# Optimization experiments

Measured on AMD Instinct MI355X. Metric: run time of the kernel, lower is better.

The kernel has to match this reference:

```python
import jax, jax.numpy as jnp
import numpy as np

R, N, F_IN, F_OUT = 8, 40000, 128, 128
E = 160000  # edges per relation


def setup_inputs() -> dict:
    key = jax.random.key(0)
    ks = jax.random.split(key, 10)
    ent_mat = jax.random.normal(ks[0], (N, F_IN), dtype=jnp.float32)
    rel_mat = jax.random.normal(ks[1], (R, F_IN), dtype=jnp.float32)
    edge_src = jax.random.randint(ks[2], (R, E), 0, N, dtype=jnp.int32)
    edge_dst = jax.random.randint(ks[3], (R, E), 0, N, dtype=jnp.int32)
    edge_val = jax.random.uniform(ks[4], (R, E), dtype=jnp.float32)
    # learned params (xavier-ish scale)
    s_e = (6.0 / (F_IN + F_OUT)) ** 0.5
    weight_ent = jax.random.uniform(ks[5], (F_IN, F_OUT), minval=-s_e, maxval=s_e, dtype=jnp.float32)
    proj_w1 = jax.random.uniform(ks[6], (F_IN, F_OUT), minval=-s_e, maxval=s_e, dtype=jnp.float32)
    proj_b1 = jnp.zeros((F_OUT,), dtype=jnp.float32)
    s_2 = (6.0 / (F_OUT + 1)) ** 0.5
    proj_w2 = jax.random.uniform(ks[7], (F_OUT, 1), minval=-s_2, maxval=s_2, dtype=jnp.float32)
    return {"ent_mat": ent_mat, "rel_mat": rel_mat, "edge_src": edge_src,
            "edge_dst": edge_dst, "edge_val": edge_val, "weight_ent": weight_ent,
            "proj_w1": proj_w1, "proj_b1": proj_b1, "proj_w2": proj_w2}


def reference(ent_mat, rel_mat, edge_src, edge_dst, edge_val, weight_ent, proj_w1, proj_b1, proj_w2):
    # Per-relation SpMM: supports[r] = A_r @ ent_mat, via edge-list segment-sum.
    seg = (jnp.arange(R, dtype=jnp.int32)[:, None] * N + edge_src).reshape(-1)  # [R*E]
    msgs = edge_val.reshape(-1, 1) * ent_mat[edge_dst.reshape(-1)]              # [R*E, F_IN]
    supports = jax.ops.segment_sum(msgs, seg, num_segments=R * N).reshape(R, N, F_IN)
    # Relation gate: sigmoid(Linear(Tanh(Linear(rel_mat))))
    h = jnp.tanh(rel_mat @ proj_w1 + proj_b1)      # [R, F_OUT]
    alpha = jax.nn.sigmoid(h @ proj_w2)            # [R, 1]
    alpha = alpha[:, None, :]                      # [R, 1, 1]
    # Weighted matmul + sum over relations (fused via einsum)
    ent_output = jnp.einsum('rnf,fo->no', supports * alpha, weight_ent)  # [N, F_OUT]
    return (ent_output, rel_mat)
```

## Files before the change

kernel.cpp:

```cpp
#include <hip/hip_runtime.h>

#define R_ 8
#define N_ 40000
#define F_ 128
#define E_ 160000
#define NE (R_ * E_)
#define NBUK 625
#define CAP 2560
#define FBLK 320
#define FCHUNK 4000
#define RELCHUNKS (E_ / FCHUNK)

typedef unsigned short ushort;
typedef unsigned int uint;
typedef __attribute__((ext_vector_type(8))) short bf16x8;
typedef __attribute__((ext_vector_type(4))) float f32x4;

__device__ __forceinline__ ushort f2bf(float x) {
    uint u = __float_as_uint(x);
    return (ushort)((u + 0x7fffu + ((u >> 16) & 1u)) >> 16);
}

__global__ __launch_bounds__(256) void fused_prep(
        const float* __restrict__ ent, const float* __restrict__ W,
        ushort* __restrict__ proj,
        const int* __restrict__ esrc,
        const float* __restrict__ rel, float* __restrict__ out_tail,
        const float* __restrict__ w1, const float* __restrict__ b1,
        const float* __restrict__ w2, float* __restrict__ alpha,
        int* __restrict__ hist) {
    __shared__ float smem[64 * F_];
    const int t = threadIdx.x;
    const int b = blockIdx.x;
    if (b < 625) {
        ushort* Wt = (ushort*)smem;
#pragma unroll
        for (int p = 0; p < 16; ++p) {
            int k = p * 8 + (t >> 5);
            int c4 = (t & 31) * 4;
            float4 wv = *(const float4*)&W[k * F_ + c4];
#pragma unroll
            for (int i = 0; i < 4; ++i) {
                int col = c4 + i;
                float v = (i == 0) ? wv.x : (i == 1) ? wv.y : (i == 2) ? wv.z : wv.w;
                Wt[col * F_ + ((((k >> 3) ^ (col & 7)) << 3) | (k & 7))] = f2bf(v);
            }
        }
        __syncthreads();
        const int wv_ = t >> 6;
        const int lane = t & 63;
        const int m = lane & 15;
        const int q = (lane >> 4) & 3;
        const int row0 = b * 64 + wv_ * 16;
        bf16x8 afrag[4];
        const float* arow = ent + (size_t)(row0 + m) * F_;
#pragma unroll
        for (int kc = 0; kc < 4; ++kc) {
            float4 a0 = *(const float4*)&arow[kc * 32 + q * 8];
            float4 a1 = *(const float4*)&arow[kc * 32 + q * 8 + 4];
            bf16x8 a;
            a[0] = (short)f2bf(a0.x); a[1] = (short)f2bf(a0.y);
            a[2] = (short)f2bf(a0.z); a[3] = (short)f2bf(a0.w);
            a[4] = (short)f2bf(a1.x); a[5] = (short)f2bf(a1.y);
            a[6] = (short)f2bf(a1.z); a[7] = (short)f2bf(a1.w);
            afrag[kc] = a;
        }
        f32x4 acc[8];
#pragma unroll
        for (int ct = 0; ct < 8; ++ct) acc[ct] = (f32x4){0.f, 0.f, 0.f, 0.f};
#pragma unroll
        for (int ct = 0; ct < 8; ++ct) {
            int n = ct * 16 + m;
#pragma unroll
            for (int kc = 0; kc < 4; ++kc) {
                int chunk = kc * 4 + q;
                bf16x8 bfrag = *(const bf16x8*)&Wt[n * F_ + ((chunk ^ (n & 7)) << 3)];
                acc[ct] = __builtin_amdgcn_mfma_f32_16x16x32_bf16(afrag[kc], bfrag, acc[ct], 0, 0, 0);
            }
        }
#pragma unroll
        for (int ct = 0; ct < 8; ++ct) {
#pragma unroll
            for (int reg = 0; reg < 4; ++reg) {
                int row = row0 + q * 4 + reg;
                proj[(size_t)row * F_ + ct * 16 + m] = f2bf(acc[ct][reg]);
            }
        }
    } else if (b == 625) {
        ((float4*)out_tail)[t] = ((const float4*)rel)[t];
    } else if (b < 630) {
        int r = (b - 626) * 2 + (t >> 7);
        int o = t & 127;
        float s = 0.f;
#pragma unroll 8
        for (int f = 0; f < F_; ++f) s += rel[r * F_ + f] * w1[f * F_ + o];
        float h = tanhf(s + b1[o]);
        smem[t] = h * w2[o];
        __syncthreads();
        for (int off = 64; off > 0; off >>= 1) {
            if ((t & 127) < off) smem[t] += smem[t + off];
            __syncthreads();
        }
        if ((t & 127) == 0) alpha[r] = 1.f / (1.f + expf(-smem[t]));
    } else {
        int hb = b - 630;
        int* h = (int*)smem;
        for (int i = t; i < NBUK; i += 256) h[i] = 0;
        __syncthreads();
        int base = hb * FCHUNK;
        for (int i = t; i < FCHUNK; i += 256)
            atomicAdd(&h[esrc[base + i] >> 6], 1);
        __syncthreads();
        for (int i = t; i < NBUK; i += 256) hist[hb * NBUK + i] = h[i];
    }
}

__global__ __launch_bounds__(256) void fillscan_kernel(const int* __restrict__ hist,
                                                       int* __restrict__ blockbase,
                                                       int* __restrict__ total) {
    int wv = (blockIdx.x * 256 + threadIdx.x) >> 6;
    int lane = threadIdx.x & 63;
    if (wv >= NBUK) return;
    int carry = 0;
#pragma unroll
    for (int c = 0; c < FBLK / 64; ++c) {
        int idx = c * 64 + lane;
        int v = hist[(size_t)idx * NBUK + wv];
        int s = v;
#pragma unroll
        for (int off = 1; off < 64; off <<= 1) {
            int u = __shfl_up(s, off, 64);
            if (lane >= off) s += u;
        }
        blockbase[wv * FBLK + idx] = carry + s - v;
        carry += __shfl(s, 63, 64);
    }
    if (lane == 63) total[wv] = carry;
}

__global__ __launch_bounds__(1024) void fillB_kernel(const int* __restrict__ esrc,
                                                     const int* __restrict__ edst,
                                                     const float* __restrict__ eval_,
                                                     const float* __restrict__ alpha,
                                                     const int* __restrict__ blockbase,
                                                     uint2* __restrict__ staged) {
    __shared__ int lcnt[NBUK];
    __shared__ int lbase[NBUK];
    int t = threadIdx.x, blk = blockIdx.x;
    for (int i = t; i < NBUK; i += 1024) {
        lcnt[i] = 0;
        lbase[i] = i * CAP + blockbase[i * FBLK + blk];
    }
    __syncthreads();
    const float av = alpha[blk / RELCHUNKS];
    int base = blk * FCHUNK;
    for (int i = t; i < FCHUNK; i += 1024) {
        int e = base + i;
        int s = esrc[e];
        int d = edst[e];
        float w = av * eval_[e];
        int bk = s >> 6;
        int rank = atomicAdd(&lcnt[bk], 1);
        int pos = lbase[bk] + rank;
        if (pos < (bk + 1) * CAP)
            staged[pos] = make_uint2((uint)d | ((uint)f2bf(w) << 16), (uint)s);
    }
}

__global__ __launch_bounds__(1024) void fillC_spmm(const uint2* __restrict__ staged,
                                                   const int* __restrict__ total,
                                                   const ushort* __restrict__ proj,
                                                   float* __restrict__ out) {
    __shared__ uint2 raw[CAP];
    __shared__ uint  srt[CAP];
    __shared__ int cnt[64], cur[64], rs[65];
    const int b = blockIdx.x, t = threadIdx.x;
    int n = total[b];
    if (n > CAP) n = CAP;
    if (t < 64) cnt[t] = 0;
    __syncthreads();
    const uint2* seg = staged + (size_t)b * CAP;
    for (int i = t; i < n; i += 1024) {
        uint2 e = seg[i];
        raw[i] = e;
        atomicAdd(&cnt[e.y & 63], 1);
    }
    __syncthreads();
    if (t < 64) cur[t] = cnt[t];
    __syncthreads();
    for (int off = 1; off < 64; off <<= 1) {
        int v = (t < 64 && t >= off) ? cur[t - off] : 0;
        __syncthreads();
        if (t < 64) cur[t] += v;
        __syncthreads();
    }
    if (t < 64) {
        rs[t + 1] = cur[t];
        if (t == 0) rs[0] = 0;
        cur[t] -= cnt[t];
    }
    __syncthreads();
    for (int i = t; i < n; i += 1024) {
        uint2 e = raw[i];
        int pos = atomicAdd(&cur[e.y & 63], 1);
        srt[pos] = e.x;
    }
    __syncthreads();
    const int wv = t >> 6;
    const int lane = t & 63;
    for (int rr = 0; rr < 4; ++rr) {
        int r = wv * 4 + rr;
        int beg = rs[r], end = rs[r + 1];
        float ax0 = 0.f, ay0 = 0.f, ax1 = 0.f, ay1 = 0.f;
        int j = beg;
        for (; j + 8 <= end; j += 8) {
            uint e[8], u[8];
#pragma unroll
            for (int k = 0; k < 8; ++k) e[k] = srt[j + k];
#pragma unroll
            for (int k = 0; k < 8; ++k)
                u[k] = *(const uint*)&proj[((e[k] & 0xffffu) << 7) + 2 * lane];
#pragma unroll
            for (int k = 0; k < 8; ++k) {
                float w = __uint_as_float(e[k] & 0xffff0000u);
                if (k & 1) {
                    ax1 += w * __uint_as_float(u[k] << 16);
                    ay1 += w * __uint_as_float(u[k] & 0xffff0000u);
                } else {
                    ax0 += w * __uint_as_float(u[k] << 16);
                    ay0 += w * __uint_as_float(u[k] & 0xffff0000u);
                }
            }
        }
        for (; j < end; ++j) {
            uint e = srt[j];
            uint u = *(const uint*)&proj[((e & 0xffffu) << 7) + 2 * lane];
            float w = __uint_as_float(e & 0xffff0000u);
            ax0 += w * __uint_as_float(u << 16);
            ay0 += w * __uint_as_float(u & 0xffff0000u);
        }
        *(float2*)&out[(((size_t)b * 64 + r) << 7) + 2 * lane] =
            make_float2(ax0 + ax1, ay0 + ay1);
    }
}

extern "C" void kernel_launch(void* const* d_in, const int* in_sizes, int n_in,
                              void* d_out, int out_size, void* d_ws, size_t ws_size,
                              hipStream_t stream) {
    const float* ent   = (const float*)d_in[0];
    const float* rel   = (const float*)d_in[1];
    const int*   esrc  = (const int*)d_in[2];
    const int*   edst  = (const int*)d_in[3];
    const float* eval_ = (const float*)d_in[4];
    const float* went  = (const float*)d_in[5];
    const float* w1    = (const float*)d_in[6];
    const float* b1    = (const float*)d_in[7];
    const float* w2    = (const float*)d_in[8];

    float* out      = (float*)d_out;
    float* out_tail = out + (size_t)N_ * F_;

    char* ws = (char*)d_ws;
    size_t off = 0;
    ushort* proj      = (ushort*)(ws + off); off += (size_t)N_ * F_ * 2;
    uint2*  staged    = (uint2*)(ws + off);  off += (size_t)NBUK * CAP * 8;
    float*  alpha     = (float*)(ws + off);  off += 256;
    int*    hist      = (int*)(ws + off);    off += (size_t)FBLK * NBUK * 4;
    int*    blockbase = (int*)(ws + off);    off += (size_t)NBUK * FBLK * 4;
    int*    total     = (int*)(ws + off);    off += (size_t)(NBUK + 7) * 4;

    fused_prep<<<950, 256, 0, stream>>>(ent, went, proj, esrc,
                                        rel, out_tail, w1, b1, w2, alpha, hist);
    fillscan_kernel<<<(NBUK + 3) / 4, 256, 0, stream>>>(hist, blockbase, total);
    fillB_kernel<<<FBLK, 1024, 0, stream>>>(esrc, edst, eval_, alpha, blockbase, staged);
    fillC_spmm<<<NBUK, 1024, 0, stream>>>(staged, total, proj, out);
}
```

Measured before the change: 176.6 us.

## Tile scan through LDS, transpose blockbase layout, use nontemporal memory ops, shrink blocks

The scan kernel now loads tiles of the histogram into shared memory and processes 16 buckets per block. It writes blockbase in the same row-major [block][bucket] layout as hist, so the fill kernel reads it coalesced. Nontemporal loads and stores are added for the streaming edge arrays, staged data, entity rows and output. Block sizes drop from 1024 to 256 threads for fillB and to 512 for fillC, which doubles each wave's row count in the SpMM and trades parallelism per block for occupancy.

```diff
diff --git a/kernel.cpp b/kernel.cpp
--- a/kernel.cpp
+++ b/kernel.cpp
@@ -10,9 +10,11 @@
 #define FBLK 320
 #define FCHUNK 4000
 #define RELCHUNKS (E_ / FCHUNK)
+#define FSTILE 16
 
 typedef unsigned short ushort;
 typedef unsigned int uint;
+typedef unsigned long long u64;
 typedef __attribute__((ext_vector_type(8))) short bf16x8;
 typedef __attribute__((ext_vector_type(4))) float f32x4;
 
@@ -56,13 +58,13 @@
         const float* arow = ent + (size_t)(row0 + m) * F_;
 #pragma unroll
         for (int kc = 0; kc < 4; ++kc) {
-            float4 a0 = *(const float4*)&arow[kc * 32 + q * 8];
-            float4 a1 = *(const float4*)&arow[kc * 32 + q * 8 + 4];
+            f32x4 a0 = __builtin_nontemporal_load((const f32x4*)&arow[kc * 32 + q * 8]);
+            f32x4 a1 = __builtin_nontemporal_load((const f32x4*)&arow[kc * 32 + q * 8 + 4]);
             bf16x8 a;
-            a[0] = (short)f2bf(a0.x); a[1] = (short)f2bf(a0.y);
-            a[2] = (short)f2bf(a0.z); a[3] = (short)f2bf(a0.w);
-            a[4] = (short)f2bf(a1.x); a[5] = (short)f2bf(a1.y);
-            a[6] = (short)f2bf(a1.z); a[7] = (short)f2bf(a1.w);
+            a[0] = (short)f2bf(a0[0]); a[1] = (short)f2bf(a0[1]);
+            a[2] = (short)f2bf(a0[2]); a[3] = (short)f2bf(a0[3]);
+            a[4] = (short)f2bf(a1[0]); a[5] = (short)f2bf(a1[1]);
+            a[6] = (short)f2bf(a1[2]); a[7] = (short)f2bf(a1[3]);
             afrag[kc] = a;
         }
         f32x4 acc[8];
@@ -118,47 +120,66 @@
 __global__ __launch_bounds__(256) void fillscan_kernel(const int* __restrict__ hist,
                                                        int* __restrict__ blockbase,
                                                        int* __restrict__ total) {
-    int wv = (blockIdx.x * 256 + threadIdx.x) >> 6;
-    int lane = threadIdx.x & 63;
-    if (wv >= NBUK) return;
-    int carry = 0;
-#pragma unroll
-    for (int c = 0; c < FBLK / 64; ++c) {
-        int idx = c * 64 + lane;
-        int v = hist[(size_t)idx * NBUK + wv];
-        int s = v;
-#pragma unroll
-        for (int off = 1; off < 64; off <<= 1) {
-            int u = __shfl_up(s, off, 64);
-            if (lane >= off) s += u;
-        }
-        blockbase[wv * FBLK + idx] = carry + s - v;
-        carry += __shfl(s, 63, 64);
-    }
-    if (lane == 63) total[wv] = carry;
-}
-
-__global__ __launch_bounds__(1024) void fillB_kernel(const int* __restrict__ esrc,
-                                                     const int* __restrict__ edst,
-                                                     const float* __restrict__ eval_,
-                                                     const float* __restrict__ alpha,
-                                                     const int* __restrict__ blockbase,
-                                                     uint2* __restrict__ staged) {
+    __shared__ int sc[FBLK][FSTILE + 1];
+    __shared__ int tot_s[FSTILE];
+    const int t = threadIdx.x;
+    const int tb = blockIdx.x * FSTILE;
+    for (int i = t; i < FBLK * FSTILE; i += 256) {
+        int f = i >> 4;
+        int c = i & (FSTILE - 1);
+        int bk = tb + c;
+        sc[f][c] = (bk < NBUK) ? hist[f * NBUK + bk] : 0;
+    }
+    __syncthreads();
+    const int wv = t >> 6, lane = t & 63;
+    for (int c = wv; c < FSTILE; c += 4) {
+        int carry = 0;
+#pragma unroll
+        for (int seg = 0; seg < FBLK / 64; ++seg) {
+            int f = seg * 64 + lane;
+            int v = sc[f][c];
+            int s = v;
+#pragma unroll
+            for (int off = 1; off < 64; off <<= 1) {
+                int u = __shfl_up(s, off, 64);
+                if (lane >= off) s += u;
+            }
+            sc[f][c] = carry + s - v;
+            carry += __shfl(s, 63, 64);
+        }
+        if (lane == 0) tot_s[c] = carry;
+    }
+    __syncthreads();
+    for (int i = t; i < FBLK * FSTILE; i += 256) {
+        int f = i >> 4;
+        int c = i & (FSTILE - 1);
+        int bk = tb + c;
+        if (bk < NBUK) blockbase[f * NBUK + bk] = sc[f][c];
+    }
+    if (t < FSTILE && tb + t < NBUK) total[tb + t] = tot_s[t];
+}
+
+__global__ __launch_bounds__(256) void fillB_kernel(const int* __restrict__ esrc,
+                                                    const int* __restrict__ edst,
+                                                    const float* __restrict__ eval_,
+                                                    const float* __restrict__ alpha,
+                                                    const int* __restrict__ blockbase,
+                                                    uint2* __restrict__ staged) {
     __shared__ int lcnt[NBUK];
     __shared__ int lbase[NBUK];
     int t = threadIdx.x, blk = blockIdx.x;
-    for (int i = t; i < NBUK; i += 1024) {
+    for (int i = t; i < NBUK; i += 256) {
         lcnt[i] = 0;
-        lbase[i] = i * CAP + blockbase[i * FBLK + blk];
+        lbase[i] = i * CAP + blockbase[blk * NBUK + i];
     }
     __syncthreads();
     const float av = alpha[blk / RELCHUNKS];
     int base = blk * FCHUNK;
-    for (int i = t; i < FCHUNK; i += 1024) {
+    for (int i = t; i < FCHUNK; i += 256) {
         int e = base + i;
-        int s = esrc[e];
-        int d = edst[e];
-        float w = av * eval_[e];
+        int s = __builtin_nontemporal_load(&esrc[e]);
+        int d = __builtin_nontemporal_load(&edst[e]);
+        float w = av * __builtin_nontemporal_load(&eval_[e]);
         int bk = s >> 6;
         int rank = atomicAdd(&lcnt[bk], 1);
         int pos = lbase[bk] + rank;
@@ -167,10 +188,10 @@
     }
 }
 
-__global__ __launch_bounds__(1024) void fillC_spmm(const uint2* __restrict__ staged,
-                                                   const int* __restrict__ total,
-                                                   const ushort* __restrict__ proj,
-                                                   float* __restrict__ out) {
+__global__ __launch_bounds__(512) void fillC_spmm(const uint2* __restrict__ staged,
+                                                  const int* __restrict__ total,
+                                                  const ushort* __restrict__ proj,
+                                                  float* __restrict__ out) {
     __shared__ uint2 raw[CAP];
     __shared__ uint  srt[CAP];
     __shared__ int cnt[64], cur[64], rs[65];
@@ -179,9 +200,10 @@
     if (n > CAP) n = CAP;
     if (t < 64) cnt[t] = 0;
     __syncthreads();
-    const uint2* seg = staged + (size_t)b * CAP;
-    for (int i = t; i < n; i += 1024) {
-        uint2 e = seg[i];
+    const u64* seg64 = (const u64*)(staged + (size_t)b * CAP);
+    for (int i = t; i < n; i += 512) {
+        u64 v = __builtin_nontemporal_load(&seg64[i]);
+        uint2 e = make_uint2((uint)v, (uint)(v >> 32));
         raw[i] = e;
         atomicAdd(&cnt[e.y & 63], 1);
     }
@@ -200,7 +222,7 @@
         cur[t] -= cnt[t];
     }
     __syncthreads();
-    for (int i = t; i < n; i += 1024) {
+    for (int i = t; i < n; i += 512) {
         uint2 e = raw[i];
         int pos = atomicAdd(&cur[e.y & 63], 1);
         srt[pos] = e.x;
@@ -208,8 +230,8 @@
     __syncthreads();
     const int wv = t >> 6;
     const int lane = t & 63;
-    for (int rr = 0; rr < 4; ++rr) {
-        int r = wv * 4 + rr;
+    for (int rr = 0; rr < 8; ++rr) {
+        int r = wv * 8 + rr;
         int beg = rs[r], end = rs[r + 1];
         float ax0 = 0.f, ay0 = 0.f, ax1 = 0.f, ay1 = 0.f;
         int j = beg;
@@ -239,8 +261,9 @@
             ax0 += w * __uint_as_float(u << 16);
             ay0 += w * __uint_as_float(u & 0xffff0000u);
         }
-        *(float2*)&out[(((size_t)b * 64 + r) << 7) + 2 * lane] =
-            make_float2(ax0 + ax1, ay0 + ay1);
+        u64 pv = ((u64)__float_as_uint(ay0 + ay1) << 32) | (u64)__float_as_uint(ax0 + ax1);
+        __builtin_nontemporal_store(pv,
+            (u64*)&out[(((size_t)b * 64 + r) << 7) + 2 * lane]);
     }
 }
 
@@ -266,12 +289,12 @@
     uint2*  staged    = (uint2*)(ws + off);  off += (size_t)NBUK * CAP * 8;
     float*  alpha     = (float*)(ws + off);  off += 256;
     int*    hist      = (int*)(ws + off);    off += (size_t)FBLK * NBUK * 4;
-    int*    blockbase = (int*)(ws + off);    off += (size_t)NBUK * FBLK * 4;
+    int*    blockbase = (int*)(ws + off);    off += (size_t)FBLK * NBUK * 4;
     int*    total     = (int*)(ws + off);    off += (size_t)(NBUK + 7) * 4;
 
     fused_prep<<<950, 256, 0, stream>>>(ent, went, proj, esrc,
                                         rel, out_tail, w1, b1, w2, alpha, hist);
-    fillscan_kernel<<<(NBUK + 3) / 4, 256, 0, stream>>>(hist, blockbase, total);
-    fillB_kernel<<<FBLK, 1024, 0, stream>>>(esrc, edst, eval_, alpha, blockbase, staged);
-    fillC_spmm<<<NBUK, 1024, 0, stream>>>(staged, total, proj, out);
-}
+    fillscan_kernel<<<(NBUK + FSTILE - 1) / FSTILE, 256, 0, stream>>>(hist, blockbase, total);
+    fillB_kernel<<<FBLK, 256, 0, stream>>>(esrc, edst, eval_, alpha, blockbase, staged);
+    fillC_spmm<<<NBUK, 512, 0, stream>>>(staged, total, proj, out);
+}
```

New measurement: 192.0 us. 1.09x slower.
